# Kernel tuning notes

Measured on AMD Instinct MI355X. Metric: run time of the kernel, lower is better.

The kernel has to match this reference:

```python
import jax, jax.numpy as jnp
import numpy as np

DIM = 1024
N_HEADS = 16
N_KV_HEADS = 4
HEAD_DIM = 64
BATCH = 1
SEQ = 4096
ROPE_BASE = 1000.0


def _rope_tables(seq_len, head_dim, base):
    theta = 1.0 / base ** (jnp.arange(0, head_dim, 2, dtype=jnp.float32) / head_dim)
    freqs = jnp.outer(jnp.arange(seq_len, dtype=jnp.float32), theta)  # [S, hd/2]
    return jnp.cos(freqs), jnp.sin(freqs)


def _apply_rope(x, cos, sin):
    # x: [B, S, H, hd]; cos/sin: [S, hd/2] -> broadcast [1, S, 1, hd/2]
    c = cos[None, :, None, :]
    s = sin[None, :, None, :]
    x1, x2 = x[..., ::2], x[..., 1::2]
    even = x1 * c - x2 * s
    odd = x1 * s + x2 * c
    return jnp.stack([even, odd], axis=-1).reshape(x.shape)


def setup_inputs() -> dict:
    key = jax.random.key(0)
    kx, kq, kk, kv, ko = jax.random.split(key, 5)
    x = jax.random.normal(kx, (BATCH, SEQ, DIM), dtype=jnp.float32)
    # causal mask (1 = attend, 0 = masked)
    mask = jnp.tril(jnp.ones((SEQ, SEQ), dtype=jnp.int32))[None, None, :, :]
    scale = DIM ** -0.5
    Wq = jax.random.normal(kq, (DIM, N_HEADS * HEAD_DIM), dtype=jnp.float32) * scale
    Wk = jax.random.normal(kk, (DIM, N_KV_HEADS * HEAD_DIM), dtype=jnp.float32) * scale
    Wv = jax.random.normal(kv, (DIM, N_KV_HEADS * HEAD_DIM), dtype=jnp.float32) * scale
    Wo = jax.random.normal(ko, (N_HEADS * HEAD_DIM, DIM), dtype=jnp.float32) * scale
    return {"x": x, "mask": mask, "Wq": Wq, "Wk": Wk, "Wv": Wv, "Wo": Wo}


def reference(x, mask, Wq, Wk, Wv, Wo):
    batch, seq_len, _ = x.shape
    q = (x @ Wq).reshape(batch, seq_len, N_HEADS, HEAD_DIM)
    k = (x @ Wk).reshape(batch, seq_len, N_KV_HEADS, HEAD_DIM)
    v = (x @ Wv).reshape(batch, seq_len, N_KV_HEADS, HEAD_DIM)
    cos, sin = _rope_tables(seq_len, HEAD_DIM, ROPE_BASE)
    q = _apply_rope(q, cos, sin)
    k = _apply_rope(k, cos, sin)
    rep = N_HEADS // N_KV_HEADS
    k = jnp.repeat(k, rep, axis=2)  # [B, S, H, hd]
    v = jnp.repeat(v, rep, axis=2)
    q = q.transpose(0, 2, 1, 3)  # [B, H, S, hd]
    k = k.transpose(0, 2, 1, 3)
    v = v.transpose(0, 2, 1, 3)
    scale = HEAD_DIM ** -0.5
    scores = jnp.einsum('bhqd,bhkd->bhqk', q, k) * scale  # [B, H, S, S]
    scores = jnp.where(mask == 0, -jnp.inf, scores)
    attn = jax.nn.softmax(scores, axis=-1)
    out = jnp.einsum('bhqk,bhkd->bhqd', attn, v)
    out = out.transpose(0, 2, 1, 3).reshape(batch, seq_len, N_HEADS * HEAD_DIM)
    return out @ Wo
```

## Files before the change

### kernel.cpp

```cpp
#include <hip/hip_runtime.h>
#include <hip/hip_bf16.h>

typedef __attribute__((ext_vector_type(8))) short short8;
typedef __attribute__((ext_vector_type(4))) float f32x4;
typedef unsigned short u16;
typedef unsigned int u32;

#define SEQ 4096

__device__ __forceinline__ u16 f2bf(float f) {
  return __builtin_bit_cast(u16, __float2bfloat16(f));
}

#if __has_builtin(__builtin_amdgcn_exp2f)
#define EXP2(x) __builtin_amdgcn_exp2f(x)
#else
#define EXP2(x) exp2f(x)
#endif

__device__ __forceinline__ u32 pk2(float a, float b) {
  u32 ua = __builtin_bit_cast(u32, a) + 0x8000u;
  u32 ub = __builtin_bit_cast(u32, b) + 0x8000u;
  return __builtin_amdgcn_perm(ub, ua, 0x07060302);
}

__device__ __forceinline__ u32 pk2t(float a, float b) {
  return __builtin_amdgcn_perm(__builtin_bit_cast(u32, b),
                               __builtin_bit_cast(u32, a), 0x07060302);
}

typedef __attribute__((address_space(1))) u32 gas_u32;
typedef __attribute__((address_space(3))) u32 las_u32;
__device__ __forceinline__ void gload16(const u16* g, const u16* l) {
  __builtin_amdgcn_global_load_lds((gas_u32*)(unsigned long long)(const void*)g,
                                   (las_u32*)(u32)(unsigned long long)(const void*)l,
                                   16, 0, 0);
}

#define VM_DRAIN() asm volatile("s_waitcnt vmcnt(0)" ::: "memory")

__global__ __launch_bounds__(256) void k_prep(const float* __restrict__ x,
                                              u16* __restrict__ xb,
                                              float* __restrict__ cosT,
                                              float* __restrict__ sinT) {
  int bid = blockIdx.x;
  if (bid < 4096) {
    int i = bid * 256 + threadIdx.x;
    float4 v = ((const float4*)x)[i];
    u32 lo = (u32)f2bf(v.x) | ((u32)f2bf(v.y) << 16);
    u32 hi = (u32)f2bf(v.z) | ((u32)f2bf(v.w) << 16);
    uint2 o; o.x = lo; o.y = hi;
    ((uint2*)xb)[i] = o;
  } else {
    int tid = (bid - 4096) * 256 + threadIdx.x;
    int pos = tid >> 5, j = tid & 31;
    float theta = exp2f(-0.311430758895f * (float)j);
    float a = (float)pos * theta;
    float s, c;
    sincosf(a, &s, &c);
    cosT[tid] = c;
    sinT[tid] = s;
  }
}

__global__ __launch_bounds__(256) void k_tconvW(const float* __restrict__ Wq,
                                                const float* __restrict__ Wk,
                                                const float* __restrict__ Wv,
                                                const float* __restrict__ Wo,
                                                u16* __restrict__ Wt,
                                                u16* __restrict__ Wto) {
  __shared__ float tile[64][65];
  int bid = blockIdx.x;
  const float* src; u16* dst; int sstride, bx, by;
  if (bid < 256)      { src = Wq; dst = Wt;              sstride = 1024; bx = bid & 15;        by = bid >> 4; }
  else if (bid < 320) { src = Wk; dst = Wt + 1024 * 1024; sstride = 256;  bx = (bid - 256) & 3; by = (bid - 256) >> 2; }
  else if (bid < 384) { src = Wv; dst = Wt + 1280 * 1024; sstride = 256;  bx = (bid - 320) & 3; by = (bid - 320) >> 2; }
  else                { src = Wo; dst = Wto;             sstride = 1024; bx = (bid - 384) & 15; by = (bid - 384) >> 4; }
  const int dstride = 1024;
  int br = by * 64, bc = bx * 64;
  int t = threadIdx.x;
#pragma unroll
  for (int i = 0; i < 16; ++i) {
    int idx = t + i * 256;
    int r = idx >> 6, c = idx & 63;
    tile[r][c] = src[(long)(br + r) * sstride + bc + c];
  }
  __syncthreads();
#pragma unroll
  for (int i = 0; i < 16; ++i) {
    int idx = t + i * 256;
    int cc = idx >> 6, rr = idx & 63;
    dst[(long)(bc + cc) * dstride + br + rr] = f2bf(tile[rr][cc]);
  }
}

__global__ __launch_bounds__(256) void k_gemm(const u16* __restrict__ A,
                                              const u16* __restrict__ Bt,
                                              float* __restrict__ C,
                                              int M, int N, int K) {
  __shared__ __align__(16) u16 a_lds[128 * 64];
  __shared__ __align__(16) u16 b_lds[64 * 64];
  const int bm = blockIdx.x * 128, bn = blockIdx.y * 64;
  const int t = threadIdx.x;
  const int l = t & 63, w = t >> 6;
  const int wm = (w >> 1) * 64, wn = (w & 1) * 32;
  const int lg = l >> 4, ll = l & 15;

  const f32x4 vzero = {0.f, 0.f, 0.f, 0.f};
  f32x4 acc[4][2];
#pragma unroll
  for (int i = 0; i < 4; ++i)
#pragma unroll
    for (int j = 0; j < 2; ++j) acc[i][j] = vzero;

  const u16* ga = A + (long)(bm + w * 32 + (l >> 3)) * K + (l & 7) * 8;
  const u16* gb = Bt + (long)(bn + w * 16 + (l >> 3)) * K + (l & 7) * 8;
  u16* la = a_lds + w * 32 * 64;
  u16* lb = b_lds + w * 16 * 64;
  const long rstep = (long)8 * K;

  for (int kt = 0; kt < K; kt += 64) {
    __syncthreads();
#pragma unroll
    for (int i = 0; i < 4; ++i) gload16(ga + i * rstep, la + i * 512);
#pragma unroll
    for (int i = 0; i < 2; ++i) gload16(gb + i * rstep, lb + i * 512);
    ga += 64; gb += 64;
    __syncthreads();
#pragma unroll
    for (int kc = 0; kc < 2; ++kc) {
      short8 af[4], bfr[2];
#pragma unroll
      for (int mi = 0; mi < 4; ++mi)
        af[mi] = *(const short8*)(a_lds + (wm + mi * 16 + ll) * 64 + kc * 32 + lg * 8);
#pragma unroll
      for (int nb = 0; nb < 2; ++nb)
        bfr[nb] = *(const short8*)(b_lds + (wn + nb * 16 + ll) * 64 + kc * 32 + lg * 8);
#pragma unroll
      for (int mi = 0; mi < 4; ++mi)
#pragma unroll
        for (int nb = 0; nb < 2; ++nb)
          acc[mi][nb] = __builtin_amdgcn_mfma_f32_16x16x32_bf16(af[mi], bfr[nb],
                                                                acc[mi][nb], 0, 0, 0);
    }
  }
  const int rbase = bm + wm + lg * 4;
  const int cbase = bn + wn + ll;
#pragma unroll
  for (int mi = 0; mi < 4; ++mi)
#pragma unroll
    for (int nb = 0; nb < 2; ++nb)
#pragma unroll
      for (int r = 0; r < 4; ++r)
        C[(long)(rbase + mi * 16 + r) * N + cbase + nb * 16] = acc[mi][nb][r];
}

__global__ __launch_bounds__(256) void k_gemmqkv(const u16* __restrict__ A,
                                                 const u16* __restrict__ Bt,
                                                 const float* __restrict__ cosT,
                                                 const float* __restrict__ sinT,
                                                 u16* __restrict__ qb,
                                                 u16* __restrict__ kb,
                                                 u16* __restrict__ vb) {
  const int K = 1024;
  __shared__ __align__(16) u16 a_lds[128 * 64];
  __shared__ __align__(16) u16 b_lds[64 * 64];
  const int bm = blockIdx.x * 128, bn = blockIdx.y * 64;
  const int t = threadIdx.x;
  const int l = t & 63, w = t >> 6;
  const int wm = (w >> 1) * 64, wn = (w & 1) * 32;
  const int lg = l >> 4, ll = l & 15;

  const f32x4 vzero = {0.f, 0.f, 0.f, 0.f};
  f32x4 acc[4][2];
#pragma unroll
  for (int i = 0; i < 4; ++i)
#pragma unroll
    for (int j = 0; j < 2; ++j) acc[i][j] = vzero;

  const u16* ga = A + (long)(bm + w * 32 + (l >> 3)) * K + (l & 7) * 8;
  const u16* gb = Bt + (long)(bn + w * 16 + (l >> 3)) * K + (l & 7) * 8;
  u16* la = a_lds + w * 32 * 64;
  u16* lb = b_lds + w * 16 * 64;
  const long rstep = (long)8 * K;

  for (int kt = 0; kt < K; kt += 64) {
    __syncthreads();
#pragma unroll
    for (int i = 0; i < 4; ++i) gload16(ga + i * rstep, la + i * 512);
#pragma unroll
    for (int i = 0; i < 2; ++i) gload16(gb + i * rstep, lb + i * 512);
    ga += 64; gb += 64;
    __syncthreads();
#pragma unroll
    for (int kc = 0; kc < 2; ++kc) {
      short8 af[4], bfr[2];
#pragma unroll
      for (int mi = 0; mi < 4; ++mi)
        af[mi] = *(const short8*)(a_lds + (wm + mi * 16 + ll) * 64 + kc * 32 + lg * 8);
#pragma unroll
      for (int nb = 0; nb < 2; ++nb)
        bfr[nb] = *(const short8*)(b_lds + (wn + nb * 16 + ll) * 64 + kc * 32 + lg * 8);
#pragma unroll
      for (int mi = 0; mi < 4; ++mi)
#pragma unroll
        for (int nb = 0; nb < 2; ++nb)
          acc[mi][nb] = __builtin_amdgcn_mfma_f32_16x16x32_bf16(af[mi], bfr[nb],
                                                                acc[mi][nb], 0, 0, 0);
    }
  }

  const int rbase = bm + wm + lg * 4;
  const int cbase = bn + wn + ll;
  const int by = blockIdx.y;

  if (by < 20) {
    const float scale = (by < 16) ? 0.18033688011112042f : 1.0f;
#pragma unroll
    for (int mi = 0; mi < 4; ++mi)
#pragma unroll
      for (int nb = 0; nb < 2; ++nb) {
        int col = cbase + nb * 16;
        int j = (col & 63) >> 1;
        long hb = (by < 16) ? (long)(col >> 6) * SEQ
                            : (long)((col - 1024) >> 6) * SEQ;
        u16* dst0 = ((by < 16) ? qb : kb) + hb * 64 + (col & 63);
#pragma unroll
        for (int r = 0; r < 4; ++r) {
          float v0 = acc[mi][nb][r];
          float vp = __shfl_xor(v0, 1);
          int row = rbase + mi * 16 + r;
          float c = cosT[(row << 5) + j], s = sinT[(row << 5) + j];
          float res = (ll & 1) ? (vp * s + v0 * c) * scale
                               : (v0 * c - vp * s) * scale;
          dst0[(long)row * 64] = f2bf(res);
        }
      }
  } else {
#pragma unroll
    for (int mi = 0; mi < 4; ++mi)
#pragma unroll
      for (int nb = 0; nb < 2; ++nb) {
        int col = cbase + nb * 16;
        int vd = col - 1280;
        int row0 = rbase + mi * 16;
        int T = row0 & ~63;
        int kb64 = row0 & 63;
        int s0 = (kb64 & 32) + ((kb64 & 12) << 1) + ((kb64 & 16) >> 2);
        uint2 gg;
        gg.x = pk2(acc[mi][nb][0], acc[mi][nb][1]);
        gg.y = pk2(acc[mi][nb][2], acc[mi][nb][3]);
        *(uint2*)(vb + (long)vd * SEQ + T + s0) = gg;
      }
  }
}

__global__ __launch_bounds__(128) void k_attn(const u16* __restrict__ q,
                                              const u16* __restrict__ kk,
                                              const u16* __restrict__ vT,
                                              u16* __restrict__ o) {
  const int b = blockIdx.x;
  const int h = b & 15;
  const int qt = 63 - (b >> 4);
  const int hkv = h >> 2;
  __shared__ __align__(16) u16 kbuf[2][64 * 64];
  __shared__ __align__(16) u16 vbuf[2][64 * 64];
  __shared__ float lsm[2][64];
  const int t = threadIdx.x, w = t >> 6, l = t & 63;
  const int lg = l >> 4, ll = l & 15;
  const f32x4 vzero = {0.f, 0.f, 0.f, 0.f};
  const short8 vones = {0x3F80, 0x3F80, 0x3F80, 0x3F80,
                        0x3F80, 0x3F80, 0x3F80, 0x3F80};

  const int r16 = t >> 3, c8 = t & 7;
  const int cswz = c8 ^ (r16 & 7);
  const u16* kbase = kk + (long)hkv * SEQ * 64;
  const u16* vbase = vT + (long)hkv * 64 * SEQ;
  const u16* kcur = kbase + (long)r16 * 64 + cswz * 8;
  const u16* vc0 = vbase + (long)r16 * SEQ + cswz * 8;
  const u16* vc1 = vc0 + (long)16 * SEQ;
  const u16* vc2 = vc0 + (long)32 * SEQ;
  const u16* vc3 = vc0 + (long)48 * SEQ;
  const int ldst = r16 * 64 + c8 * 8;

  const int kwbyte = w * 32 * 128;
  const int rbyte = ll * 128;
  const int g0 = (lg ^ (ll & 7)) << 4;
  const int g1 = ((lg ^ (ll & 7)) ^ 4) << 4;
  const int gv = ((w * 4 + lg) ^ (ll & 7)) << 4;

#define ISSUE(BUF)                                                           \
  {                                                                          \
    u16* kld = kbuf[BUF] + ldst;                                             \
    u16* vld = vbuf[BUF] + ldst;                                             \
    gload16(kcur, kld);              gload16(kcur + 1024, kld + 1024);       \
    gload16(kcur + 2048, kld + 2048); gload16(kcur + 3072, kld + 3072);      \
    gload16(vc0, vld);               gload16(vc1, vld + 1024);               \
    gload16(vc2, vld + 2048);        gload16(vc3, vld + 3072);               \
    kcur += 4096; vc0 += 64; vc1 += 64; vc2 += 64; vc3 += 64;                \
  }

  ISSUE(0);
  int buf = 0;

  const int q0 = qt * 64;
  short8 qa[4][2];
#pragma unroll
  for (int g = 0; g < 4; ++g)
#pragma unroll
    for (int c = 0; c < 2; ++c)
      qa[g][c] = *(const short8*)(q + ((long)(h * SEQ + q0 + g * 16 + ll) * 64 +
                                       c * 32 + lg * 8));

  f32x4 Oacc[4][4];
#pragma unroll
  for (int g = 0; g < 4; ++g)
#pragma unroll
    for (int nb = 0; nb < 4; ++nb) Oacc[g][nb] = vzero;
  f32x4 lsum[4] = {vzero, vzero, vzero, vzero};

  for (int kt = 0; kt <= qt; ++kt) {
    VM_DRAIN();
    __syncthreads();
    if (kt < qt) { ISSUE(buf ^ 1); }

    const char* kb_ = (const char*)kbuf[buf] + kwbyte + rbyte;
    const char* vb_ = (const char*)vbuf[buf] + rbyte;

    f32x4 S[2][4];
    __builtin_amdgcn_s_setprio(1);
#pragma unroll
    for (int st = 0; st < 2; ++st) {
      short8 ka0 = *(const short8*)(kb_ + st * 2048 + g0);
      short8 ka1 = *(const short8*)(kb_ + st * 2048 + g1);
#pragma unroll
      for (int g = 0; g < 4; ++g) {
        f32x4 z = __builtin_amdgcn_mfma_f32_16x16x32_bf16(ka0, qa[g][0], vzero, 0, 0, 0);
        S[st][g] = __builtin_amdgcn_mfma_f32_16x16x32_bf16(ka1, qa[g][1], z, 0, 0, 0);
      }
    }
    __builtin_amdgcn_s_setprio(0);

    if (kt == qt) {
#pragma unroll
      for (int st = 0; st < 2; ++st)
#pragma unroll
        for (int g = 0; g < 4; ++g)
#pragma unroll
          for (int r = 0; r < 4; ++r)
            if (w * 32 + st * 16 + lg * 4 + r > g * 16 + ll)
              S[st][g][r] = -__builtin_inff();
    }

    short8 vv[4];
#pragma unroll
    for (int nb = 0; nb < 4; ++nb)
      vv[nb] = *(const short8*)(vb_ + nb * 2048 + gv);

#pragma unroll
    for (int g = 0; g < 4; ++g) {
      float p00 = EXP2(S[0][g][0]), p01 = EXP2(S[0][g][1]);
      float p02 = EXP2(S[0][g][2]), p03 = EXP2(S[0][g][3]);
      float p10 = EXP2(S[1][g][0]), p11 = EXP2(S[1][g][1]);
      float p12 = EXP2(S[1][g][2]), p13 = EXP2(S[1][g][3]);
      uint4 u;
      u.x = pk2t(p00, p01); u.y = pk2t(p02, p03);
      u.z = pk2t(p10, p11); u.w = pk2t(p12, p13);
      short8 pa = __builtin_bit_cast(short8, u);
      __builtin_amdgcn_s_setprio(1);
      lsum[g] = __builtin_amdgcn_mfma_f32_16x16x32_bf16(pa, vones, lsum[g], 0, 0, 0);
      Oacc[g][0] = __builtin_amdgcn_mfma_f32_16x16x32_bf16(pa, vv[0], Oacc[g][0], 0, 0, 0);
      Oacc[g][1] = __builtin_amdgcn_mfma_f32_16x16x32_bf16(pa, vv[1], Oacc[g][1], 0, 0, 0);
      Oacc[g][2] = __builtin_amdgcn_mfma_f32_16x16x32_bf16(pa, vv[2], Oacc[g][2], 0, 0, 0);
      Oacc[g][3] = __builtin_amdgcn_mfma_f32_16x16x32_bf16(pa, vv[3], Oacc[g][3], 0, 0, 0);
      __builtin_amdgcn_s_setprio(0);
    }
    buf ^= 1;
  }
#undef ISSUE

  __syncthreads();
  float* myO = w ? (float*)vbuf : (float*)kbuf;
#pragma unroll
  for (int g = 0; g < 4; ++g)
#pragma unroll
    for (int nb = 0; nb < 4; ++nb)
#pragma unroll
      for (int r = 0; r < 4; ++r)
        myO[(g * 16 + lg * 4 + r) * 64 + nb * 16 + ll] = Oacc[g][nb][r];
  if (ll == 0) {
#pragma unroll
    for (int g = 0; g < 4; ++g)
#pragma unroll
      for (int r = 0; r < 4; ++r)
        lsm[w][g * 16 + lg * 4 + r] = lsum[g][r];
  }
  __syncthreads();
  const float* O0 = (const float*)kbuf;
  const float* O1 = (const float*)vbuf;
#pragma unroll 4
  for (int qq = 0; qq < 32; ++qq) {
    int qr = w * 32 + qq;
    float v = O0[qr * 64 + l] + O1[qr * 64 + l];
    float inv = 1.f / (lsm[0][qr] + lsm[1][qr]);
    o[(long)(q0 + qr) * 1024 + h * 64 + l] = f2bf(v * inv);
  }
}

extern "C" void kernel_launch(void* const* d_in, const int* in_sizes, int n_in,
                              void* d_out, int out_size, void* d_ws, size_t ws_size,
                              hipStream_t stream) {
  const float* x  = (const float*)d_in[0];
  const float* Wq = (const float*)d_in[2];
  const float* Wk = (const float*)d_in[3];
  const float* Wv = (const float*)d_in[4];
  const float* Wo = (const float*)d_in[5];
  float* out = (float*)d_out;

  char* ws = (char*)d_ws;
  u16* xb    = (u16*)(ws + 25165824);
  u16* Wt    = (u16*)(ws + 33554432);
  u16* Wto   = (u16*)(ws + 36700160);
  u16* qb    = (u16*)(ws + 38797312);
  u16* kb    = (u16*)(ws + 47185920);
  u16* vb    = (u16*)(ws + 49283072);
  float* cosT = (float*)(ws + 51380224);
  float* sinT = (float*)(ws + 51904512);

  k_prep<<<4608, 256, 0, stream>>>(x, xb, cosT, sinT);
  k_tconvW<<<640, 256, 0, stream>>>(Wq, Wk, Wv, Wo, Wt, Wto);

  k_gemmqkv<<<dim3(32, 24), 256, 0, stream>>>(xb, Wt, cosT, sinT, qb, kb, vb);

  k_attn<<<1024, 128, 0, stream>>>(qb, kb, vb, xb);

  k_gemm<<<dim3(32, 16), 256, 0, stream>>>(xb, Wto, out, 4096, 1024, 1024);
}
```

Baseline: 120.3 us.

## Split attention block across four waves over query and key halves

The attention kernel now launches 256 threads per block instead of 128. Its four waves split the 64x64 tile into query halves and key halves, so each wave holds half as many query rows and accumulators. The tile loads are spread over four waves, and the final merge writes 16 rows per wave. This adds more waves per block to hide latency and cuts per-wave register use, at the cost of more block-level synchronisation and shared-memory contention per tile.

```diff
diff --git a/kernel.cpp b/kernel.cpp
--- a/kernel.cpp
+++ b/kernel.cpp
@@ -255,7 +255,7 @@
   }
 }
 
-__global__ __launch_bounds__(128) void k_attn(const u16* __restrict__ q,
+__global__ __launch_bounds__(256) void k_attn(const u16* __restrict__ q,
                                               const u16* __restrict__ kk,
                                               const u16* __restrict__ vT,
                                               u16* __restrict__ o) {
@@ -268,56 +268,52 @@
   __shared__ float lsm[2][64];
   const int t = threadIdx.x, w = t >> 6, l = t & 63;
   const int lg = l >> 4, ll = l & 15;
+  const int wq = w >> 1, wk = w & 1;
   const f32x4 vzero = {0.f, 0.f, 0.f, 0.f};
   const short8 vones = {0x3F80, 0x3F80, 0x3F80, 0x3F80,
                         0x3F80, 0x3F80, 0x3F80, 0x3F80};
 
-  const int r16 = t >> 3, c8 = t & 7;
-  const int cswz = c8 ^ (r16 & 7);
+  const int lr = l >> 3, lc = l & 7;
+  const int cswz = lc ^ (lr & 7);
   const u16* kbase = kk + (long)hkv * SEQ * 64;
   const u16* vbase = vT + (long)hkv * 64 * SEQ;
-  const u16* kcur = kbase + (long)r16 * 64 + cswz * 8;
-  const u16* vc0 = vbase + (long)r16 * SEQ + cswz * 8;
-  const u16* vc1 = vc0 + (long)16 * SEQ;
-  const u16* vc2 = vc0 + (long)32 * SEQ;
-  const u16* vc3 = vc0 + (long)48 * SEQ;
-  const int ldst = r16 * 64 + c8 * 8;
-
-  const int kwbyte = w * 32 * 128;
+  const u16* kcur  = kbase + (long)(w * 16 + lr) * 64 + cswz * 8;
+  const u16* vcurA = vbase + (long)(w * 16 + lr) * SEQ + cswz * 8;
+  const u16* vcurB = vcurA + (long)8 * SEQ;
+
   const int rbyte = ll * 128;
   const int g0 = (lg ^ (ll & 7)) << 4;
   const int g1 = ((lg ^ (ll & 7)) ^ 4) << 4;
-  const int gv = ((w * 4 + lg) ^ (ll & 7)) << 4;
+  const int gv = ((wk * 4 + lg) ^ (ll & 7)) << 4;
+  const int kwbyte = wk * 32 * 128;
 
 #define ISSUE(BUF)                                                           \
   {                                                                          \
-    u16* kld = kbuf[BUF] + ldst;                                             \
-    u16* vld = vbuf[BUF] + ldst;                                             \
-    gload16(kcur, kld);              gload16(kcur + 1024, kld + 1024);       \
-    gload16(kcur + 2048, kld + 2048); gload16(kcur + 3072, kld + 3072);      \
-    gload16(vc0, vld);               gload16(vc1, vld + 1024);               \
-    gload16(vc2, vld + 2048);        gload16(vc3, vld + 3072);               \
-    kcur += 4096; vc0 += 64; vc1 += 64; vc2 += 64; vc3 += 64;                \
+    u16* kld = kbuf[BUF] + w * 1024;                                         \
+    u16* vld = vbuf[BUF] + w * 1024;                                         \
+    gload16(kcur, kld);          gload16(kcur + 512, kld + 512);             \
+    gload16(vcurA, vld);         gload16(vcurB, vld + 512);                  \
+    kcur += 4096; vcurA += 64; vcurB += 64;                                  \
   }
 
   ISSUE(0);
   int buf = 0;
 
   const int q0 = qt * 64;
-  short8 qa[4][2];
-#pragma unroll
-  for (int g = 0; g < 4; ++g)
+  short8 qa[2][2];
+#pragma unroll
+  for (int g = 0; g < 2; ++g)
 #pragma unroll
     for (int c = 0; c < 2; ++c)
-      qa[g][c] = *(const short8*)(q + ((long)(h * SEQ + q0 + g * 16 + ll) * 64 +
+      qa[g][c] = *(const short8*)(q + ((long)(h * SEQ + q0 + wq * 32 + g * 16 + ll) * 64 +
                                        c * 32 + lg * 8));
 
-  f32x4 Oacc[4][4];
-#pragma unroll
-  for (int g = 0; g < 4; ++g)
+  f32x4 Oacc[2][4];
+#pragma unroll
+  for (int g = 0; g < 2; ++g)
 #pragma unroll
     for (int nb = 0; nb < 4; ++nb) Oacc[g][nb] = vzero;
-  f32x4 lsum[4] = {vzero, vzero, vzero, vzero};
+  f32x4 lsum[2] = {vzero, vzero};
 
   for (int kt = 0; kt <= qt; ++kt) {
     VM_DRAIN();
@@ -327,14 +323,14 @@
     const char* kb_ = (const char*)kbuf[buf] + kwbyte + rbyte;
     const char* vb_ = (const char*)vbuf[buf] + rbyte;
 
-    f32x4 S[2][4];
+    f32x4 S[2][2];
     __builtin_amdgcn_s_setprio(1);
 #pragma unroll
     for (int st = 0; st < 2; ++st) {
       short8 ka0 = *(const short8*)(kb_ + st * 2048 + g0);
       short8 ka1 = *(const short8*)(kb_ + st * 2048 + g1);
 #pragma unroll
-      for (int g = 0; g < 4; ++g) {
+      for (int g = 0; g < 2; ++g) {
         f32x4 z = __builtin_amdgcn_mfma_f32_16x16x32_bf16(ka0, qa[g][0], vzero, 0, 0, 0);
         S[st][g] = __builtin_amdgcn_mfma_f32_16x16x32_bf16(ka1, qa[g][1], z, 0, 0, 0);
       }
@@ -345,10 +341,10 @@
 #pragma unroll
       for (int st = 0; st < 2; ++st)
 #pragma unroll
-        for (int g = 0; g < 4; ++g)
+        for (int g = 0; g < 2; ++g)
 #pragma unroll
           for (int r = 0; r < 4; ++r)
-            if (w * 32 + st * 16 + lg * 4 + r > g * 16 + ll)
+            if (wk * 32 + st * 16 + lg * 4 + r > wq * 32 + g * 16 + ll)
               S[st][g][r] = -__builtin_inff();
     }
 
@@ -358,7 +354,7 @@
       vv[nb] = *(const short8*)(vb_ + nb * 2048 + gv);
 
 #pragma unroll
-    for (int g = 0; g < 4; ++g) {
+    for (int g = 0; g < 2; ++g) {
       float p00 = EXP2(S[0][g][0]), p01 = EXP2(S[0][g][1]);
       float p02 = EXP2(S[0][g][2]), p03 = EXP2(S[0][g][3]);
       float p10 = EXP2(S[1][g][0]), p11 = EXP2(S[1][g][1]);
@@ -380,27 +376,27 @@
 #undef ISSUE
 
   __syncthreads();
-  float* myO = w ? (float*)vbuf : (float*)kbuf;
-#pragma unroll
-  for (int g = 0; g < 4; ++g)
+  float* myO = wk ? (float*)vbuf : (float*)kbuf;
+#pragma unroll
+  for (int g = 0; g < 2; ++g)
 #pragma unroll
     for (int nb = 0; nb < 4; ++nb)
 #pragma unroll
       for (int r = 0; r < 4; ++r)
-        myO[(g * 16 + lg * 4 + r) * 64 + nb * 16 + ll] = Oacc[g][nb][r];
+        myO[(wq * 32 + g * 16 + lg * 4 + r) * 64 + nb * 16 + ll] = Oacc[g][nb][r];
   if (ll == 0) {
 #pragma unroll
-    for (int g = 0; g < 4; ++g)
+    for (int g = 0; g < 2; ++g)
 #pragma unroll
       for (int r = 0; r < 4; ++r)
-        lsm[w][g * 16 + lg * 4 + r] = lsum[g][r];
+        lsm[wk][wq * 32 + g * 16 + lg * 4 + r] = lsum[g][r];
   }
   __syncthreads();
   const float* O0 = (const float*)kbuf;
   const float* O1 = (const float*)vbuf;
 #pragma unroll 4
-  for (int qq = 0; qq < 32; ++qq) {
-    int qr = w * 32 + qq;
+  for (int qq = 0; qq < 16; ++qq) {
+    int qr = w * 16 + qq;
     float v = O0[qr * 64 + l] + O1[qr * 64 + l];
     float inv = 1.f / (lsm[0][qr] + lsm[1][qr]);
     o[(long)(q0 + qr) * 1024 + h * 64 + l] = f2bf(v * inv);
@@ -432,7 +428,7 @@
 
   k_gemmqkv<<<dim3(32, 24), 256, 0, stream>>>(xb, Wt, cosT, sinT, qb, kb, vb);
 
-  k_attn<<<1024, 128, 0, stream>>>(qb, kb, vb, xb);
+  k_attn<<<1024, 256, 0, stream>>>(qb, kb, vb, xb);
 
   k_gemm<<<dim3(32, 16), 256, 0, stream>>>(xb, Wto, out, 4096, 1024, 1024);
 }
```

New measurement: 107.4 us. 10.7% less time.
